# Optimization experiments

Hardware: AMD Instinct MI355X
Metric: run time of the kernel (lower is better)

Reference implementation:

```python
import jax, jax.numpy as jnp
import numpy as np

K = 20
EPS = 1e-5
NEG_SLOPE = 0.2


def knn(x, k):
    # x: [B, C, N] -> idx [B, N, k] of nearest neighbors (negative sq-dist topk)
    inner = -2.0 * jnp.einsum('bcn,bcm->bnm', x, x)
    xx = jnp.sum(x * x, axis=1)  # [B, N]
    d = -xx[:, :, None] - inner - xx[:, None, :]
    return jax.lax.top_k(d, k)[1]


def get_graph_feature(x, k):
    # x: [B, C, N] -> [B, 2C, N, k]
    idx = knn(x, k)
    xt = jnp.transpose(x, (0, 2, 1))            # [B, N, C]
    feat = jax.vmap(lambda a, i: a[i])(xt, idx)  # [B, N, k, C]
    center = xt[:, :, None, :]
    out = jnp.concatenate([feat - center, jnp.broadcast_to(center, feat.shape)], axis=-1)
    return jnp.transpose(out, (0, 3, 1, 2))


def conv_bn_lrelu(x, w, g, b):
    # 1x1 conv + BatchNorm2d (batch stats, training mode) + LeakyReLU(0.2)
    y = jnp.einsum('oc,bcnk->bonk', w, x)
    mu = jnp.mean(y, axis=(0, 2, 3), keepdims=True)
    var = jnp.mean((y - mu) ** 2, axis=(0, 2, 3), keepdims=True)
    y = (y - mu) * jax.lax.rsqrt(var + EPS)
    y = y * g[None, :, None, None] + b[None, :, None, None]
    return jnp.where(y >= 0, y, NEG_SLOPE * y)


def lrelu(y):
    return jnp.where(y >= 0, y, NEG_SLOPE * y)


def setup_inputs() -> dict:
    key = jax.random.key(0)
    ks = jax.random.split(key, 24)
    B, N = 8, 4096
    d = {}
    d['x'] = jax.random.normal(ks[0], (B, 3, N), dtype=jnp.float32)
    def wconv(k_, o, c):
        return jax.random.normal(k_, (o, c), dtype=jnp.float32) * (1.0 / np.sqrt(c))
    d['w1'] = wconv(ks[1], 32, 6)
    d['g1'] = 1.0 + 0.1 * jax.random.normal(ks[2], (32,), dtype=jnp.float32)
    d['b1'] = 0.1 * jax.random.normal(ks[3], (32,), dtype=jnp.float32)
    d['w2'] = wconv(ks[4], 64, 70)
    d['g2'] = 1.0 + 0.1 * jax.random.normal(ks[5], (64,), dtype=jnp.float32)
    d['b2'] = 0.1 * jax.random.normal(ks[6], (64,), dtype=jnp.float32)
    d['wd1'] = wconv(ks[7], 64, 64)
    d['gd1'] = 1.0 + 0.1 * jax.random.normal(ks[8], (64,), dtype=jnp.float32)
    d['bd1'] = 0.1 * jax.random.normal(ks[9], (64,), dtype=jnp.float32)
    d['wd2'] = wconv(ks[10], 64, 128)
    d['gd2'] = 1.0 + 0.1 * jax.random.normal(ks[11], (64,), dtype=jnp.float32)
    d['bd2'] = 0.1 * jax.random.normal(ks[12], (64,), dtype=jnp.float32)
    d['W2d'] = jax.random.normal(ks[13], (128, 128), dtype=jnp.float32) * (1.0 / np.sqrt(128))
    d['b2d'] = 0.1 * jax.random.normal(ks[14], (128,), dtype=jnp.float32)
    d['W3d'] = jax.random.normal(ks[15], (64, 128), dtype=jnp.float32) * (1.0 / np.sqrt(128))
    d['b3d'] = 0.1 * jax.random.normal(ks[16], (64,), dtype=jnp.float32)
    d['W4d'] = jax.random.normal(ks[17], (11, 64), dtype=jnp.float32) * (1.0 / np.sqrt(64))
    d['b4d'] = 0.1 * jax.random.normal(ks[18], (11,), dtype=jnp.float32)
    return d


def reference(x, w1, g1, b1, w2, g2, b2, wd1, gd1, bd1, wd2, gd2, bd2,
              W2d, b2d, W3d, b3d, W4d, b4d):
    x1_gf = get_graph_feature(x, K)                    # [B, 6, N, k]
    x1_max = jnp.max(conv_bn_lrelu(x1_gf, w1, g1, b1), axis=-1)  # [B, 32, N]
    x2_gf = jnp.concatenate([x1_gf, get_graph_feature(x1_max, K)], axis=1)  # [B, 70, N, k]
    x2_max = jnp.max(conv_bn_lrelu(x2_gf, w2, g2, b2), axis=-1)  # [B, 64, N]
    xd1 = jnp.max(conv_bn_lrelu(get_graph_feature(x1_max, K), wd1, gd1, bd1), axis=-1)  # [B, 64, N]
    xd2 = jnp.max(conv_bn_lrelu(get_graph_feature(x2_max, K), wd2, gd2, bd2), axis=-1)  # [B, 64, N]
    h = jnp.concatenate([xd1, xd2], axis=1)            # [B, 128, N]
    h = h.reshape(1, -1, 128)                          # faithful row-major view
    h = jnp.mean(h, axis=1)                            # [1, 128]
    h = lrelu(h @ W2d.T + b2d)
    h = lrelu(h @ W3d.T + b3d)
    return lrelu(h @ W4d.T + b4d)                      # [1, 11]
```

## Files before the change

### kernel.cpp

```cpp
#include <hip/hip_runtime.h>

#define BB 8
#define NN 4096
#define KK 20
constexpr float EPSV = 1e-5f;
constexpr float SLOPE = 0.2f;

typedef __bf16 bfrag __attribute__((ext_vector_type(8)));
typedef float floatx4 __attribute__((ext_vector_type(4)));
typedef unsigned short us4 __attribute__((ext_vector_type(4)));
typedef unsigned short us8 __attribute__((ext_vector_type(8)));

__device__ __forceinline__ float lrelu(float v) { return v >= 0.f ? v : SLOPE * v; }

__device__ __forceinline__ unsigned short bf16rn(float f) {
    unsigned int u = __float_as_uint(f);
    return (unsigned short)((u + 0x7FFFu + ((u >> 16) & 1u)) >> 16);
}
__device__ __forceinline__ float bf16up(unsigned short h) {
    return __uint_as_float(((unsigned int)h) << 16);
}

__global__ void zero_kernel(float* p, int n) {
    int i = blockIdx.x * 256 + threadIdx.x;
    if (i < n) p[i] = 0.f;
}

template<int C>
__global__ void halfnorm_kernel(const float* __restrict__ src, float* __restrict__ hng) {
    int n = blockIdx.x * 256 + threadIdx.x;
    int b = blockIdx.y;
    float s = 0.f;
    #pragma unroll
    for (int c = 0; c < C; c++) { float v = src[(b * C + c) * NN + n]; s += v * v; }
    hng[b * NN + n] = 0.5f * s;
}

template<int C>
__global__ void pack_kernel(const float* __restrict__ src, unsigned short* __restrict__ pk) {
    constexpr int SK = 2 * C + 8;
    const int b = blockIdx.y;
    const int m0 = blockIdx.x * 64;
    const int tid = threadIdx.x;
    for (int i = tid; i < 64 * (C / 4); i += 256) {
        int m = i & 63;
        int c4 = (i >> 6) * 4;
        us4 hv, lv;
        #pragma unroll
        for (int j = 0; j < 4; j++) {
            float v = src[(b * C + c4 + j) * NN + m0 + m];
            unsigned short h = bf16rn(v);
            hv[j] = h;
            lv[j] = bf16rn(v - bf16up(h));
        }
        *(us4*)(&pk[(size_t)(b * NN + m0 + m) * SK + c4]) = hv;
        *(us4*)(&pk[(size_t)(b * NN + m0 + m) * SK + C + c4]) = lv;
    }
    for (int i = tid; i < 64 * 2; i += 256) {
        int m = i >> 1, p = (i & 1) * 4;
        *(us4*)(&pk[(size_t)(b * NN + m0 + m) * SK + 2 * C + p]) = (us4)(0);
    }
}

__global__ void pack3_kernel(const float* __restrict__ src, unsigned short* __restrict__ pk) {
    const int b = blockIdx.y;
    const int m = blockIdx.x * 256 + threadIdx.x;
    us8 w0, w1;
    #pragma unroll
    for (int j = 0; j < 8; j++) { w0[j] = 0; w1[j] = 0; }
    unsigned short row[12];
    #pragma unroll
    for (int c = 0; c < 3; c++) {
        float v = src[(b * 3 + c) * NN + m];
        unsigned short h = bf16rn(v);
        unsigned short l = bf16rn(v - bf16up(h));
        row[c] = h; row[3 + c] = l; row[6 + c] = l; row[9 + c] = h;
    }
    #pragma unroll
    for (int j = 0; j < 8; j++) w0[j] = row[j];
    #pragma unroll
    for (int j = 0; j < 4; j++) w1[j] = row[8 + j];
    unsigned short* dst = pk + (size_t)(b * NN + m) * 40;
    us8 z;
    #pragma unroll
    for (int j = 0; j < 8; j++) z[j] = 0;
    *(us8*)(dst) = w0;
    *(us8*)(dst + 8) = w1;
    *(us8*)(dst + 16) = z;
    *(us8*)(dst + 24) = z;
    *(us8*)(dst + 32) = z;
}

template<int C>
__global__ __launch_bounds__(256) void knn_kernel(const float* __restrict__ src,
                                                  const unsigned short* __restrict__ pk,
                                                  const float* __restrict__ hng,
                                                  int* __restrict__ idx) {
    constexpr int SK = (C == 3) ? 40 : (2 * C + 8);
    constexpr int UNITS = 8 * SK;
    constexpr int PF = (UNITS + 255) / 256;
    constexpr int KKN = (C == 3) ? 1 : (C / 32);
    __shared__ __attribute__((aligned(16))) unsigned short cpack[64 * SK];
    __shared__ float pv[64 * 65];
    __shared__ unsigned short pidx[64 * 66];
    __shared__ float hn[64];
    __shared__ float tau[64];
    __shared__ int cnt[64];
    __shared__ unsigned short qls[(C == 3) ? 64 * 40 : 2];

    const int bid = blockIdx.x;
    const int b = bid & 7;
    const int q0 = (bid >> 3) * 64;
    const int tid = threadIdx.x;
    const int lane = tid & 63;
    const int wv = tid >> 6;
    const int wr = (wv >> 1) * 32;
    const int wc = (wv & 1) * 32;
    const int fl = lane & 15;
    const int fq = lane >> 4;

    float tv[20]; int ti[20];
    #pragma unroll
    for (int k = 0; k < 20; k++) { tv[k] = -3.4e38f; ti[k] = 0; }

    bfrag qah[KKN][2], qal[KKN][2];
    if (C == 3) {
        for (int i = tid; i < 64 * 20; i += 256) {
            int r = i / 20, k = 12 + i % 20;
            qls[r * 40 + k] = 0;
        }
        if (tid < 64) {
            #pragma unroll
            for (int c = 0; c < 3; c++) {
                float v = src[(b * 3 + c) * NN + q0 + tid];
                unsigned short h = bf16rn(v);
                unsigned short l = bf16rn(v - bf16up(h));
                qls[tid * 40 + c] = h;  qls[tid * 40 + 3 + c] = l;
                qls[tid * 40 + 6 + c] = h;  qls[tid * 40 + 9 + c] = l;
            }
        }
    } else {
        #pragma unroll
        for (int r2 = 0; r2 < 2; r2++) {
            const unsigned short* qr = pk + (size_t)(b * NN + q0 + wr + r2 * 16 + fl) * SK + fq * 8;
            #pragma unroll
            for (int kk = 0; kk < KKN; kk++) {
                qah[kk][r2] = *(const bfrag*)(qr + kk * 32);
                qal[kk][r2] = *(const bfrag*)(qr + C + kk * 32);
            }
        }
    }

    {
        const unsigned short* p0 = pk + (size_t)(b * NN) * SK;
        #pragma unroll
        for (int r = 0; r < PF; r++) {
            int u = r * 256 + tid;
            if (u < UNITS) *(us8*)(cpack + u * 8) = *(const us8*)(p0 + u * 8);
        }
    }
    us8 pf[PF];
    {
        const unsigned short* p1 = pk + (size_t)(b * NN + 64) * SK;
        #pragma unroll
        for (int r = 0; r < PF; r++) {
            int u = r * 256 + tid;
            if (u < UNITS) pf[r] = *(const us8*)(p1 + u * 8);
        }
    }
    float hnf = 0.f;
    if (tid < 64) {
        hn[tid] = hng[b * NN + tid];
        hnf = hng[b * NN + 64 + tid];
        tau[tid] = -3.4e38f;
        cnt[tid] = 0;
    }
    __syncthreads();

    bfrag qa3[2];
    if (C == 3) {
        #pragma unroll
        for (int r2 = 0; r2 < 2; r2++)
            qa3[r2] = *(const bfrag*)(&qls[(wr + r2 * 16 + fl) * 40 + fq * 8]);
    }

    for (int ch = 0; ch < 64; ch++) {
        if (ch > 0) {
            #pragma unroll
            for (int r = 0; r < PF; r++) {
                int u = r * 256 + tid;
                if (u < UNITS) *(us8*)(cpack + u * 8) = pf[r];
            }
            if (tid < 64) hn[tid] = hnf;
        }
        if (ch + 1 < 64) {
            const unsigned short* pn = pk + (size_t)(b * NN + (ch + 1) * 64) * SK;
            #pragma unroll
            for (int r = 0; r < PF; r++) {
                int u = r * 256 + tid;
                if (u < UNITS) pf[r] = *(const us8*)(pn + u * 8);
            }
            if (tid < 64) hnf = hng[b * NN + (ch + 1) * 64 + tid];
        }
        __syncthreads();

        floatx4 acc[2][2];
        #pragma unroll
        for (int r2 = 0; r2 < 2; r2++)
            #pragma unroll
            for (int c2 = 0; c2 < 2; c2++)
                acc[r2][c2] = (floatx4)(0.f);

        if (C == 3) {
            #pragma unroll
            for (int c2 = 0; c2 < 2; c2++) {
                bfrag bm = *(const bfrag*)(&cpack[(wc + c2 * 16 + fl) * SK + fq * 8]);
                #pragma unroll
                for (int r2 = 0; r2 < 2; r2++)
                    acc[r2][c2] = __builtin_amdgcn_mfma_f32_16x16x32_bf16(qa3[r2], bm, acc[r2][c2], 0, 0, 0);
            }
        } else {
            #pragma unroll
            for (int kk = 0; kk < KKN; kk++) {
                const int kb = kk * 32 + fq * 8;
                bfrag bh[2], bl[2];
                #pragma unroll
                for (int c2 = 0; c2 < 2; c2++) {
                    bh[c2] = *(const bfrag*)(&cpack[(wc + c2 * 16 + fl) * SK + kb]);
                    bl[c2] = *(const bfrag*)(&cpack[(wc + c2 * 16 + fl) * SK + C + kb]);
                }
                #pragma unroll
                for (int r2 = 0; r2 < 2; r2++)
                    #pragma unroll
                    for (int c2 = 0; c2 < 2; c2++) {
                        acc[r2][c2] = __builtin_amdgcn_mfma_f32_16x16x32_bf16(qah[kk][r2], bh[c2], acc[r2][c2], 0, 0, 0);
                        acc[r2][c2] = __builtin_amdgcn_mfma_f32_16x16x32_bf16(qah[kk][r2], bl[c2], acc[r2][c2], 0, 0, 0);
                        acc[r2][c2] = __builtin_amdgcn_mfma_f32_16x16x32_bf16(qal[kk][r2], bh[c2], acc[r2][c2], 0, 0, 0);
                        acc[r2][c2] = __builtin_amdgcn_mfma_f32_16x16x32_bf16(qal[kk][r2], bl[c2], acc[r2][c2], 0, 0, 0);
                    }
            }
        }

        {
            const int m0 = ch * 64;
            const float hnv0 = hn[wc + fl];
            const float hnv1 = hn[wc + 16 + fl];
            #pragma unroll
            for (int r2 = 0; r2 < 2; r2++) {
                const int qb = wr + r2 * 16 + fq * 4;
                float4 t4 = *(const float4*)(&tau[qb]);
                float ta[4] = { t4.x, t4.y, t4.z, t4.w };
                #pragma unroll
                for (int c2 = 0; c2 < 2; c2++) {
                    const float hv = c2 ? hnv1 : hnv0;
                    const int mm = m0 + wc + c2 * 16 + fl;
                    #pragma unroll
                    for (int reg = 0; reg < 4; reg++) {
                        float s = acc[r2][c2][reg] - hv;
                        if (s > ta[reg]) {
                            int q = qb + reg;
                            int p = atomicAdd(&cnt[q], 1);
                            pv[q * 65 + p] = s;
                            pidx[q * 66 + p] = (unsigned short)mm;
                        }
                    }
                }
            }
        }
        __syncthreads();

        if (tid < 64) {
            int n = cnt[tid];
            for (int t = 0; t < n; t++) {
                float v = pv[tid * 65 + t];
                if (v > tv[0]) {
                    tv[0] = v; ti[0] = (int)pidx[tid * 66 + t];
                    #pragma unroll
                    for (int j = 0; j < 19; j++) {
                        if (tv[j] > tv[j + 1]) {
                            float a = tv[j]; tv[j] = tv[j + 1]; tv[j + 1] = a;
                            int bi = ti[j]; ti[j] = ti[j + 1]; ti[j + 1] = bi;
                        }
                    }
                }
            }
            cnt[tid] = 0;
            tau[tid] = tv[0];
        }
        __syncthreads();
    }

    if (tid < 64) {
        #pragma unroll
        for (int k = 0; k < 20; k++)
            idx[(b * NN + q0 + tid) * KK + k] = ti[k];
    }
}

template<int COUT>
__global__ void precompute_kernel(const float* __restrict__ src, int C,
                                  const float* __restrict__ w, int CIN, int wd_off, int wc_off,
                                  float* __restrict__ G, float* __restrict__ H,
                                  int initG, int initH) {
    constexpr int MY = 256 / COUT;
    extern __shared__ float lds[];
    float* wd = lds;
    float* wc = lds + C * COUT;
    const int b = blockIdx.y;
    const int tid = threadIdx.y * COUT + threadIdx.x;
    for (int i = tid; i < C * COUT; i += 256) {
        int c = i / COUT, o = i % COUT;
        float a  = w[o * CIN + wd_off + c];
        float cc = w[o * CIN + wc_off + c];
        wd[i] = a;
        wc[i] = cc - a;
    }
    __syncthreads();
    const int o = threadIdx.x;
    for (int it = 0; it < COUT / 4; it++) {
        int m = blockIdx.x * 64 + it * MY + threadIdx.y;
        float g = 0.f, h = 0.f;
        for (int c = 0; c < C; c++) {
            float s = src[(b * C + c) * NN + m];
            g += wd[c * COUT + o] * s;
            h += wc[c * COUT + o] * s;
        }
        int gi = (b * NN + m) * COUT + o;
        if (initG) G[gi] = g; else G[gi] += g;
        if (initH) H[gi] = h; else H[gi] += h;
    }
}

template<int COUT, int GROUPS>
__global__ void conv_stats_kernel(const float* __restrict__ G1, const int* __restrict__ idx1,
                                  const float* __restrict__ G2, const int* __restrict__ idx2,
                                  const float* __restrict__ H, float* __restrict__ stats,
                                  float* __restrict__ MaxY, float* __restrict__ MinY) {
    constexpr int NY = 256 / COUT;
    const int b = blockIdx.y;
    const int o = threadIdx.x;
    const int n = blockIdx.x * NY + threadIdx.y;
    const int base = b * NN + n;
    const float h = H[base * COUT + o];
    float s1 = 0.f, s2 = 0.f;
    float gx = -3.4e38f, gn = 3.4e38f;
    #pragma unroll
    for (int k = 0; k < KK; k++) {
        int i1 = idx1[base * KK + k];
        float g = G1[(b * NN + i1) * COUT + o];
        if (GROUPS == 2) {
            int i2 = idx2[base * KK + k];
            g += G2[(b * NN + i2) * COUT + o];
        }
        float y = g + h;
        s1 += y;
        s2 += y * y;
        gx = fmaxf(gx, g);
        gn = fminf(gn, g);
    }
    MaxY[base * COUT + o] = gx + h;
    MinY[base * COUT + o] = gn + h;

    __shared__ float ls[2 * COUT];
    if (threadIdx.y == 0) { ls[o] = 0.f; ls[COUT + o] = 0.f; }
    __syncthreads();
    atomicAdd(&ls[o], s1);
    atomicAdd(&ls[COUT + o], s2);
    __syncthreads();
    if (threadIdx.y == 0) {
        atomicAdd(&stats[o], ls[o]);
        atomicAdd(&stats[64 + o], ls[COUT + o]);
    }
}

__global__ void finalize_kernel(const float* __restrict__ g, const float* __restrict__ bb,
                                float* __restrict__ stats, int cout, float invP) {
    int o = threadIdx.x;
    if (o >= cout) return;
    float mu  = stats[o] * invP;
    float var = stats[64 + o] * invP - mu * mu;
    float sc  = g[o] * rsqrtf(var + EPSV);
    stats[128 + o] = sc;
    stats[192 + o] = bb[o] - mu * sc;
}

__global__ void apply_kernel(const float* __restrict__ MaxY, const float* __restrict__ MinY,
                             const float* __restrict__ stats, float* __restrict__ out, int cout) {
    int e = blockIdx.x * 256 + threadIdx.x;
    int total = BB * cout * NN;
    if (e >= total) return;
    int n = e & (NN - 1);
    int o = (e >> 12) % cout;
    int b = e / (NN * cout);
    float sc = stats[128 + o], sh = stats[192 + o];
    int si = (b * NN + n) * cout + o;
    float v = (sc >= 0.f) ? MaxY[si] : MinY[si];
    out[e] = lrelu(sc * v + sh);
}

__global__ void mean_kernel(const float* __restrict__ xd1, const float* __restrict__ xd2,
                            float* __restrict__ hsum) {
    __shared__ float bins[128];
    const int tid = threadIdx.x;
    if (tid < 128) bins[tid] = 0.f;
    __syncthreads();
    const int half = BB * 64 * NN;
    const int stride = gridDim.x * 256;
    for (int e = blockIdx.x * 256 + tid; e < half; e += stride)
        atomicAdd(&bins[e & 127], xd1[e]);
    for (int e = blockIdx.x * 256 + tid; e < half; e += stride)
        atomicAdd(&bins[e & 127], xd2[e]);
    __syncthreads();
    if (tid < 128) atomicAdd(&hsum[tid], bins[tid]);
}

__global__ void head_kernel(const float* __restrict__ hsum,
                            const float* __restrict__ W2d, const float* __restrict__ b2d,
                            const float* __restrict__ W3d, const float* __restrict__ b3d,
                            const float* __restrict__ W4d, const float* __restrict__ b4d,
                            float* __restrict__ out) {
    __shared__ float h[128], t1[128], t2[64];
    const int t = threadIdx.x;
    h[t] = hsum[t] * (1.f / 32768.f);
    __syncthreads();
    float a = b2d[t];
    for (int j = 0; j < 128; j++) a += W2d[t * 128 + j] * h[j];
    t1[t] = lrelu(a);
    __syncthreads();
    if (t < 64) {
        float a2 = b3d[t];
        for (int j = 0; j < 128; j++) a2 += W3d[t * 128 + j] * t1[j];
        t2[t] = lrelu(a2);
    }
    __syncthreads();
    if (t < 11) {
        float a3 = b4d[t];
        for (int j = 0; j < 64; j++) a3 += W4d[t * 64 + j] * t2[j];
        out[t] = lrelu(a3);
    }
}

extern "C" void kernel_launch(void* const* d_in, const int* in_sizes, int n_in,
                              void* d_out, int out_size, void* d_ws, size_t ws_size,
                              hipStream_t stream) {
    const float* x   = (const float*)d_in[0];
    const float* w1  = (const float*)d_in[1];
    const float* g1  = (const float*)d_in[2];
    const float* b1  = (const float*)d_in[3];
    const float* w2  = (const float*)d_in[4];
    const float* g2  = (const float*)d_in[5];
    const float* b2  = (const float*)d_in[6];
    const float* wd1 = (const float*)d_in[7];
    const float* gd1 = (const float*)d_in[8];
    const float* bd1 = (const float*)d_in[9];
    const float* wd2 = (const float*)d_in[10];
    const float* gd2 = (const float*)d_in[11];
    const float* bd2 = (const float*)d_in[12];
    const float* W2d = (const float*)d_in[13];
    const float* b2d = (const float*)d_in[14];
    const float* W3d = (const float*)d_in[15];
    const float* b3d = (const float*)d_in[16];
    const float* W4d = (const float*)d_in[17];
    const float* b4d = (const float*)d_in[18];
    float* out = (float*)d_out;

    char* ws = (char*)d_ws;
    size_t off = 0;
    auto alloc = [&](size_t bytes) { char* p = ws + off; off += (bytes + 255) & ~size_t(255); return p; };
    int*   idx1  = (int*)  alloc(BB * NN * KK * 4);
    int*   idx2  = (int*)  alloc(BB * NN * KK * 4);
    int*   idx3  = (int*)  alloc(BB * NN * KK * 4);
    float* x1m   = (float*)alloc(BB * 32 * NN * 4);
    float* x2m   = (float*)alloc(BB * 64 * NN * 4);
    float* xd1   = (float*)alloc(BB * 64 * NN * 4);
    float* xd2   = (float*)alloc(BB * 64 * NN * 4);
    float* G1    = (float*)alloc((size_t)BB * NN * 64 * 4);
    float* G2    = (float*)alloc((size_t)BB * NN * 64 * 4);
    float* H     = (float*)alloc((size_t)BB * NN * 64 * 4);
    float* MaxY  = (float*)alloc((size_t)BB * NN * 64 * 4);
    float* MinY  = (float*)alloc((size_t)BB * NN * 64 * 4);
    float* stats = (float*)alloc(256 * 4);
    float* hsum  = (float*)alloc(128 * 4);
    float* hng   = (float*)alloc(BB * NN * 4);

    unsigned short* pkbuf = (unsigned short*)MaxY;

    const float invP = 1.f / (float)(BB * NN * KK);
    const dim3 knn_grid(NN / 64 * BB);
    const dim3 hn_grid(NN / 256, BB);

    zero_kernel<<<1, 256, 0, stream>>>(hsum, 128);

    pack3_kernel<<<dim3(NN / 256, BB), 256, 0, stream>>>(x, pkbuf);
    halfnorm_kernel<3><<<hn_grid, 256, 0, stream>>>(x, hng);
    knn_kernel<3><<<knn_grid, 256, 0, stream>>>(x, pkbuf, hng, idx1);

    zero_kernel<<<1, 256, 0, stream>>>(stats, 128);
    precompute_kernel<32><<<dim3(NN / 64, BB), dim3(32, 8), 2 * 3 * 32 * 4, stream>>>(
        x, 3, w1, 6, 0, 3, G1, H, 1, 1);
    conv_stats_kernel<32, 1><<<dim3(NN / 8, BB), dim3(32, 8), 0, stream>>>(
        G1, idx1, nullptr, nullptr, H, stats, MaxY, MinY);
    finalize_kernel<<<1, 64, 0, stream>>>(g1, b1, stats, 32, invP);
    apply_kernel<<<(BB * 32 * NN + 255) / 256, 256, 0, stream>>>(MaxY, MinY, stats, x1m, 32);

    pack_kernel<32><<<dim3(NN / 64, BB), 256, 0, stream>>>(x1m, pkbuf);
    halfnorm_kernel<32><<<hn_grid, 256, 0, stream>>>(x1m, hng);
    knn_kernel<32><<<knn_grid, 256, 0, stream>>>(x1m, pkbuf, hng, idx2);

    zero_kernel<<<1, 256, 0, stream>>>(stats, 128);
    precompute_kernel<64><<<dim3(NN / 64, BB), dim3(64, 4), 2 * 3 * 64 * 4, stream>>>(
        x, 3, w2, 70, 0, 3, G1, H, 1, 1);
    precompute_kernel<64><<<dim3(NN / 64, BB), dim3(64, 4), 2 * 32 * 64 * 4, stream>>>(
        x1m, 32, w2, 70, 6, 38, G2, H, 1, 0);
    conv_stats_kernel<64, 2><<<dim3(NN / 4, BB), dim3(64, 4), 0, stream>>>(
        G1, idx1, G2, idx2, H, stats, MaxY, MinY);
    finalize_kernel<<<1, 64, 0, stream>>>(g2, b2, stats, 64, invP);
    apply_kernel<<<(BB * 64 * NN + 255) / 256, 256, 0, stream>>>(MaxY, MinY, stats, x2m, 64);

    zero_kernel<<<1, 256, 0, stream>>>(stats, 128);
    precompute_kernel<64><<<dim3(NN / 64, BB), dim3(64, 4), 2 * 32 * 64 * 4, stream>>>(
        x1m, 32, wd1, 64, 0, 32, G1, H, 1, 1);
    conv_stats_kernel<64, 1><<<dim3(NN / 4, BB), dim3(64, 4), 0, stream>>>(
        G1, idx2, nullptr, nullptr, H, stats, MaxY, MinY);
    finalize_kernel<<<1, 64, 0, stream>>>(gd1, bd1, stats, 64, invP);
    apply_kernel<<<(BB * 64 * NN + 255) / 256, 256, 0, stream>>>(MaxY, MinY, stats, xd1, 64);

    pack_kernel<64><<<dim3(NN / 64, BB), 256, 0, stream>>>(x2m, pkbuf);
    halfnorm_kernel<64><<<hn_grid, 256, 0, stream>>>(x2m, hng);
    knn_kernel<64><<<knn_grid, 256, 0, stream>>>(x2m, pkbuf, hng, idx3);

    zero_kernel<<<1, 256, 0, stream>>>(stats, 128);
    precompute_kernel<64><<<dim3(NN / 64, BB), dim3(64, 4), 2 * 64 * 64 * 4, stream>>>(
        x2m, 64, wd2, 128, 0, 64, G1, H, 1, 1);
    conv_stats_kernel<64, 1><<<dim3(NN / 4, BB), dim3(64, 4), 0, stream>>>(
        G1, idx3, nullptr, nullptr, H, stats, MaxY, MinY);
    finalize_kernel<<<1, 64, 0, stream>>>(gd2, bd2, stats, 64, invP);
    apply_kernel<<<(BB * 64 * NN + 255) / 256, 256, 0, stream>>>(MaxY, MinY, stats, xd2, 64);

    mean_kernel<<<1024, 256, 0, stream>>>(xd1, xd2, hsum);
    head_kernel<<<1, 128, 0, stream>>>(hsum, W2d, b2d, W3d, b3d, W4d, b4d, out);
}
```

Baseline: 1.756 ms.

## Double-buffer kNN candidate tiles via direct global-to-LDS loads with packed norms

The kNN kernel now uses two LDS buffers for candidate tiles and fills the next one with global_load_lds (direct global-to-LDS DMA) instead of staging through registers. The half-norms are packed into the padding slot of each packed row, so the separate hn LDS array and global loads go away. Pack kernels now run after halfnorm so they can embed the norm. This aims to overlap the next tile's load with compute and to cut register pressure and the mid-loop barrier. In exchange it doubles cpack LDS use, which may lower occupancy, and it depends on the async load landing before the single end-of-loop barrier.

```diff
diff --git a/kernel.cpp b/kernel.cpp
--- a/kernel.cpp
+++ b/kernel.cpp
@@ -21,6 +21,11 @@
     return __uint_as_float(((unsigned int)h) << 16);
 }
 
+__device__ __forceinline__ void gl_lds16(const unsigned short* g, unsigned short* l) {
+    __builtin_amdgcn_global_load_lds((const __attribute__((address_space(1))) void*)g,
+                                     (__attribute__((address_space(3))) void*)l, 16, 0, 0);
+}
+
 __global__ void zero_kernel(float* p, int n) {
     int i = blockIdx.x * 256 + threadIdx.x;
     if (i < n) p[i] = 0.f;
@@ -37,7 +42,8 @@
 }
 
 template<int C>
-__global__ void pack_kernel(const float* __restrict__ src, unsigned short* __restrict__ pk) {
+__global__ void pack_kernel(const float* __restrict__ src, const float* __restrict__ hng,
+                            unsigned short* __restrict__ pk) {
     constexpr int SK = 2 * C + 8;
     const int b = blockIdx.y;
     const int m0 = blockIdx.x * 64;
@@ -56,13 +62,19 @@
         *(us4*)(&pk[(size_t)(b * NN + m0 + m) * SK + c4]) = hv;
         *(us4*)(&pk[(size_t)(b * NN + m0 + m) * SK + C + c4]) = lv;
     }
-    for (int i = tid; i < 64 * 2; i += 256) {
-        int m = i >> 1, p = (i & 1) * 4;
-        *(us4*)(&pk[(size_t)(b * NN + m0 + m) * SK + 2 * C + p]) = (us4)(0);
-    }
-}
-
-__global__ void pack3_kernel(const float* __restrict__ src, unsigned short* __restrict__ pk) {
+    if (tid < 64) {
+        unsigned int ub = __float_as_uint(hng[b * NN + m0 + tid]);
+        us8 z;
+        #pragma unroll
+        for (int j = 0; j < 8; j++) z[j] = 0;
+        z[0] = (unsigned short)(ub & 0xFFFFu);
+        z[1] = (unsigned short)(ub >> 16);
+        *(us8*)(&pk[(size_t)(b * NN + m0 + tid) * SK + 2 * C]) = z;
+    }
+}
+
+__global__ void pack3_kernel(const float* __restrict__ src, const float* __restrict__ hng,
+                             unsigned short* __restrict__ pk) {
     const int b = blockIdx.y;
     const int m = blockIdx.x * 256 + threadIdx.x;
     us8 w0, w1;
@@ -84,26 +96,29 @@
     us8 z;
     #pragma unroll
     for (int j = 0; j < 8; j++) z[j] = 0;
+    unsigned int ub = __float_as_uint(hng[b * NN + m]);
+    us8 zh = z;
+    zh[0] = (unsigned short)(ub & 0xFFFFu);
+    zh[1] = (unsigned short)(ub >> 16);
     *(us8*)(dst) = w0;
     *(us8*)(dst + 8) = w1;
     *(us8*)(dst + 16) = z;
     *(us8*)(dst + 24) = z;
-    *(us8*)(dst + 32) = z;
+    *(us8*)(dst + 32) = zh;
 }
 
 template<int C>
 __global__ __launch_bounds__(256) void knn_kernel(const float* __restrict__ src,
                                                   const unsigned short* __restrict__ pk,
-                                                  const float* __restrict__ hng,
                                                   int* __restrict__ idx) {
     constexpr int SK = (C == 3) ? 40 : (2 * C + 8);
+    constexpr int HNOFF = (C == 3) ? 32 : 2 * C;
     constexpr int UNITS = 8 * SK;
     constexpr int PF = (UNITS + 255) / 256;
     constexpr int KKN = (C == 3) ? 1 : (C / 32);
-    __shared__ __attribute__((aligned(16))) unsigned short cpack[64 * SK];
+    __shared__ __attribute__((aligned(16))) unsigned short cpack[2 * 64 * SK];
     __shared__ float pv[64 * 65];
     __shared__ unsigned short pidx[64 * 66];
-    __shared__ float hn[64];
     __shared__ float tau[64];
     __shared__ int cnt[64];
     __shared__ unsigned short qls[(C == 3) ? 64 * 40 : 2];
@@ -155,26 +170,12 @@
         const unsigned short* p0 = pk + (size_t)(b * NN) * SK;
         #pragma unroll
         for (int r = 0; r < PF; r++) {
-            int u = r * 256 + tid;
-            if (u < UNITS) *(us8*)(cpack + u * 8) = *(const us8*)(p0 + u * 8);
-        }
-    }
-    us8 pf[PF];
-    {
-        const unsigned short* p1 = pk + (size_t)(b * NN + 64) * SK;
-        #pragma unroll
-        for (int r = 0; r < PF; r++) {
-            int u = r * 256 + tid;
-            if (u < UNITS) pf[r] = *(const us8*)(p1 + u * 8);
-        }
-    }
-    float hnf = 0.f;
-    if (tid < 64) {
-        hn[tid] = hng[b * NN + tid];
-        hnf = hng[b * NN + 64 + tid];
-        tau[tid] = -3.4e38f;
-        cnt[tid] = 0;
-    }
+            int u0 = r * 256 + wv * 64;
+            if (u0 < UNITS)
+                gl_lds16(p0 + (size_t)(u0 + lane) * 8, cpack + (size_t)u0 * 8);
+        }
+    }
+    if (tid < 64) { tau[tid] = -3.4e38f; cnt[tid] = 0; }
     __syncthreads();
 
     bfrag qa3[2];
@@ -184,25 +185,19 @@
             qa3[r2] = *(const bfrag*)(&qls[(wr + r2 * 16 + fl) * 40 + fq * 8]);
     }
 
+    int buf = 0;
     for (int ch = 0; ch < 64; ch++) {
-        if (ch > 0) {
+        unsigned short* cur = cpack + buf * (64 * SK);
+        if (ch + 1 < 64) {
+            unsigned short* nxt = cpack + (buf ^ 1) * (64 * SK);
+            const unsigned short* pn = pk + (size_t)(b * NN + (ch + 1) * 64) * SK;
             #pragma unroll
             for (int r = 0; r < PF; r++) {
-                int u = r * 256 + tid;
-                if (u < UNITS) *(us8*)(cpack + u * 8) = pf[r];
-            }
-            if (tid < 64) hn[tid] = hnf;
-        }
-        if (ch + 1 < 64) {
-            const unsigned short* pn = pk + (size_t)(b * NN + (ch + 1) * 64) * SK;
-            #pragma unroll
-            for (int r = 0; r < PF; r++) {
-                int u = r * 256 + tid;
-                if (u < UNITS) pf[r] = *(const us8*)(pn + u * 8);
-            }
-            if (tid < 64) hnf = hng[b * NN + (ch + 1) * 64 + tid];
-        }
-        __syncthreads();
+                int u0 = r * 256 + wv * 64;
+                if (u0 < UNITS)
+                    gl_lds16(pn + (size_t)(u0 + lane) * 8, nxt + (size_t)u0 * 8);
+            }
+        }
 
         floatx4 acc[2][2];
         #pragma unroll
@@ -214,7 +209,7 @@
         if (C == 3) {
             #pragma unroll
             for (int c2 = 0; c2 < 2; c2++) {
-                bfrag bm = *(const bfrag*)(&cpack[(wc + c2 * 16 + fl) * SK + fq * 8]);
+                bfrag bm = *(const bfrag*)(&cur[(wc + c2 * 16 + fl) * SK + fq * 8]);
                 #pragma unroll
                 for (int r2 = 0; r2 < 2; r2++)
                     acc[r2][c2] = __builtin_amdgcn_mfma_f32_16x16x32_bf16(qa3[r2], bm, acc[r2][c2], 0, 0, 0);
@@ -226,8 +221,8 @@
                 bfrag bh[2], bl[2];
                 #pragma unroll
                 for (int c2 = 0; c2 < 2; c2++) {
-                    bh[c2] = *(const bfrag*)(&cpack[(wc + c2 * 16 + fl) * SK + kb]);
-                    bl[c2] = *(const bfrag*)(&cpack[(wc + c2 * 16 + fl) * SK + C + kb]);
+                    bh[c2] = *(const bfrag*)(&cur[(wc + c2 * 16 + fl) * SK + kb]);
+                    bl[c2] = *(const bfrag*)(&cur[(wc + c2 * 16 + fl) * SK + C + kb]);
                 }
                 #pragma unroll
                 for (int r2 = 0; r2 < 2; r2++)
@@ -243,8 +238,10 @@
 
         {
             const int m0 = ch * 64;
-            const float hnv0 = hn[wc + fl];
-            const float hnv1 = hn[wc + 16 + fl];
+            float hvv[2];
+            #pragma unroll
+            for (int c2 = 0; c2 < 2; c2++)
+                hvv[c2] = *(const float*)(&cur[(wc + c2 * 16 + fl) * SK + HNOFF]);
             #pragma unroll
             for (int r2 = 0; r2 < 2; r2++) {
                 const int qb = wr + r2 * 16 + fq * 4;
@@ -252,7 +249,7 @@
                 float ta[4] = { t4.x, t4.y, t4.z, t4.w };
                 #pragma unroll
                 for (int c2 = 0; c2 < 2; c2++) {
-                    const float hv = c2 ? hnv1 : hnv0;
+                    const float hv = hvv[c2];
                     const int mm = m0 + wc + c2 * 16 + fl;
                     #pragma unroll
                     for (int reg = 0; reg < 4; reg++) {
@@ -288,6 +285,7 @@
             tau[tid] = tv[0];
         }
         __syncthreads();
+        buf ^= 1;
     }
 
     if (tid < 64) {
@@ -491,9 +489,9 @@
 
     zero_kernel<<<1, 256, 0, stream>>>(hsum, 128);
 
-    pack3_kernel<<<dim3(NN / 256, BB), 256, 0, stream>>>(x, pkbuf);
     halfnorm_kernel<3><<<hn_grid, 256, 0, stream>>>(x, hng);
-    knn_kernel<3><<<knn_grid, 256, 0, stream>>>(x, pkbuf, hng, idx1);
+    pack3_kernel<<<dim3(NN / 256, BB), 256, 0, stream>>>(x, hng, pkbuf);
+    knn_kernel<3><<<knn_grid, 256, 0, stream>>>(x, pkbuf, idx1);
 
     zero_kernel<<<1, 256, 0, stream>>>(stats, 128);
     precompute_kernel<32><<<dim3(NN / 64, BB), dim3(32, 8), 2 * 3 * 32 * 4, stream>>>(
@@ -503,9 +501,9 @@
     finalize_kernel<<<1, 64, 0, stream>>>(g1, b1, stats, 32, invP);
     apply_kernel<<<(BB * 32 * NN + 255) / 256, 256, 0, stream>>>(MaxY, MinY, stats, x1m, 32);
 
-    pack_kernel<32><<<dim3(NN / 64, BB), 256, 0, stream>>>(x1m, pkbuf);
     halfnorm_kernel<32><<<hn_grid, 256, 0, stream>>>(x1m, hng);
-    knn_kernel<32><<<knn_grid, 256, 0, stream>>>(x1m, pkbuf, hng, idx2);
+    pack_kernel<32><<<dim3(NN / 64, BB), 256, 0, stream>>>(x1m, hng, pkbuf);
+    knn_kernel<32><<<knn_grid, 256, 0, stream>>>(x1m, pkbuf, idx2);
 
     zero_kernel<<<1, 256, 0, stream>>>(stats, 128);
     precompute_kernel<64><<<dim3(NN / 64, BB), dim3(64, 4), 2 * 3 * 64 * 4, stream>>>(
@@ -525,9 +523,9 @@
     finalize_kernel<<<1, 64, 0, stream>>>(gd1, bd1, stats, 64, invP);
     apply_kernel<<<(BB * 64 * NN + 255) / 256, 256, 0, stream>>>(MaxY, MinY, stats, xd1, 64);
 
-    pack_kernel<64><<<dim3(NN / 64, BB), 256, 0, stream>>>(x2m, pkbuf);
     halfnorm_kernel<64><<<hn_grid, 256, 0, stream>>>(x2m, hng);
-    knn_kernel<64><<<knn_grid, 256, 0, stream>>>(x2m, pkbuf, hng, idx3);
+    pack_kernel<64><<<dim3(NN / 64, BB), 256, 0, stream>>>(x2m, hng, pkbuf);
+    knn_kernel<64><<<knn_grid, 256, 0, stream>>>(x2m, pkbuf, idx3);
 
     zero_kernel<<<1, 256, 0, stream>>>(stats, 128);
     precompute_kernel<64><<<dim3(NN / 64, BB), dim3(64, 4), 2 * 64 * 64 * 4, stream>>>(
```

Result: faster. 1.706 ms (-2.8%).
